# Optimization experiments

Measured on AMD Instinct MI355X. Metric: run time of the kernel, lower is better.

Reference implementation:

```python
import jax, jax.numpy as jnp
import numpy as np

PRED_WEIGHT = 1.0
GT_WEIGHT = 1.0
EPS = 1e-9
P = 16384
G = 16384


def setup_inputs() -> dict:
    key = jax.random.key(0)
    k1, k2, k3, k4 = jax.random.split(key, 4)
    return {
        "pred_points": jax.random.normal(k1, (P, 3), dtype=jnp.float32),
        "gt_points": jax.random.normal(k2, (G, 3), dtype=jnp.float32),
        "w_pred": jax.random.uniform(k3, (P,), dtype=jnp.float32),
        "w_gt": jax.random.uniform(k4, (G,), dtype=jnp.float32),
    }


def reference(pred_points, gt_points, w_pred, w_gt):
    # squared pairwise distances: ||p||^2 + ||g||^2 - 2 p.g, clamped at 0
    p2 = jnp.sum(pred_points * pred_points, axis=1)  # (P,)
    g2 = jnp.sum(gt_points * gt_points, axis=1)      # (G,)
    d2 = p2[:, None] + g2[None, :] - 2.0 * (pred_points @ gt_points.T)  # (P, G)
    d2 = jnp.maximum(d2, 0.0)
    min_pred = jnp.min(d2, axis=1)  # (P,)
    min_gt = jnp.min(d2, axis=0)    # (G,)
    weighted_pred = jnp.sum(w_pred * min_pred) / jnp.maximum(jnp.sum(w_pred), EPS)
    weighted_gt = jnp.sum(w_gt * min_gt) / jnp.maximum(jnp.sum(w_gt), EPS)
    return PRED_WEIGHT * weighted_pred + GT_WEIGHT * weighted_gt
```

## Files before the change

kernel.cpp:

```cpp
#include <hip/hip_runtime.h>
#include <math.h>


constexpr int NPTS  = 16384;
constexpr int BLOCK = 512;
constexpr int WAVES = BLOCK / 64;

constexpr int COLS_PER_BLOCK = 64;
constexpr int NCB = NPTS / COLS_PER_BLOCK;
constexpr int ROWS_PER_WAVE = NPTS / WAVES;
constexpr int ATILES = ROWS_PER_WAVE / 32;

typedef __attribute__((ext_vector_type(8)))  __bf16 bf16x8;
typedef __attribute__((ext_vector_type(16))) float  f32x16;

__device__ inline unsigned short f2bf(float f) {
    unsigned u = __float_as_uint(f);
    u += 0x7FFFu + ((u >> 16) & 1u);
    return (unsigned short)(u >> 16);
}
__device__ inline float bf2f(unsigned short h) {
    return __uint_as_float(((unsigned)h) << 16);
}
__device__ inline unsigned pk(unsigned short lo, unsigned short hi) {
    return (unsigned)lo | ((unsigned)hi << 16);
}

__global__ __launch_bounds__(256) void pack_init_kernel(
    const float* __restrict__ pred, const float* __restrict__ gt,
    uint4* __restrict__ Af, uint4* __restrict__ Bf,
    uint4* __restrict__ Ag, uint4* __restrict__ Bp)
{
    const unsigned short ONE = 0x3F80;
    int i = blockIdx.x * 256 + threadIdx.x;
    if (i >= NPTS) return;

    {
        float x = pred[3*i], y = pred[3*i+1], z = pred[3*i+2];
        unsigned short hx = f2bf(x), hy = f2bf(y), hz = f2bf(z);
        unsigned short lx = f2bf(x - bf2f(hx));
        unsigned short ly = f2bf(y - bf2f(hy));
        unsigned short lz = f2bf(z - bf2f(hz));
        float p2 = fmaf(x, x, fmaf(y, y, z * z));
        unsigned short sh = f2bf(p2), sl = f2bf(p2 - bf2f(sh));
        uint4 a0, a1, b0, b1;
        a0.x = pk(hx, hy); a0.y = pk(hz, lx); a0.z = pk(ly, lz); a0.w = pk(hx, hy);
        a1.x = pk(hz, sh); a1.y = pk(sl, ONE); a1.z = pk(ONE, lx); a1.w = pk(ly, lz);
        b0.x = pk(hx, hy); b0.y = pk(hz, hx); b0.z = pk(hy, hz); b0.w = pk(lx, ly);
        b1.x = pk(lz, ONE); b1.y = pk(ONE, sh); b1.z = pk(sl, lx); b1.w = pk(ly, lz);
        Af[i] = a0; Af[NPTS + i] = a1;
        Bp[i] = b0; Bp[NPTS + i] = b1;
    }
    {
        float gx = gt[3*i], gy = gt[3*i+1], gz = gt[3*i+2];
        float mx = -2.0f * gx, my = -2.0f * gy, mz = -2.0f * gz;
        unsigned short hx = f2bf(mx), hy = f2bf(my), hz = f2bf(mz);
        unsigned short lx = f2bf(mx - bf2f(hx));
        unsigned short ly = f2bf(my - bf2f(hy));
        unsigned short lz = f2bf(mz - bf2f(hz));
        float g2 = fmaf(gx, gx, fmaf(gy, gy, gz * gz));
        unsigned short sh = f2bf(g2), sl = f2bf(g2 - bf2f(sh));
        uint4 a0, a1, b0, b1;
        a0.x = pk(hx, hy); a0.y = pk(hz, lx); a0.z = pk(ly, lz); a0.w = pk(hx, hy);
        a1.x = pk(hz, sh); a1.y = pk(sl, ONE); a1.z = pk(ONE, lx); a1.w = pk(ly, lz);
        b0.x = pk(hx, hy); b0.y = pk(hz, hx); b0.z = pk(hy, hz); b0.w = pk(lx, ly);
        b1.x = pk(lz, ONE); b1.y = pk(ONE, sh); b1.z = pk(sl, lx); b1.w = pk(ly, lz);
        Ag[i] = a0; Ag[NPTS + i] = a1;
        Bf[i] = b0; Bf[NPTS + i] = b1;
    }
}

__device__ inline float tree16(const f32x16 a) {
    float m0 = fminf(fminf(a[0],  a[1]),  a[2]);
    float m1 = fminf(fminf(a[3],  a[4]),  a[5]);
    float m2 = fminf(fminf(a[6],  a[7]),  a[8]);
    float m3 = fminf(fminf(a[9],  a[10]), a[11]);
    float m4 = fminf(fminf(a[12], a[13]), a[14]);
    float m5 = fminf(fminf(m0, m1), m2);
    float m6 = fminf(fminf(m3, m4), a[15]);
    return fminf(m5, m6);
}

__global__ __launch_bounds__(BLOCK, 2) void chamfer_mfma_kernel(
    const uint4* __restrict__ Af, const uint4* __restrict__ Bf,
    const uint4* __restrict__ Ag, const uint4* __restrict__ Bp,
    const float* __restrict__ wpred, const float* __restrict__ wgt,
    float2* __restrict__ partials)
{
    const int tid  = threadIdx.x;
    const int wv   = tid >> 6;
    const int lane = tid & 63;
    const int half = lane >> 5;
    const int ln31 = lane & 31;

    const uint4* __restrict__ Aside;
    const uint4* __restrict__ Bside;
    const float* __restrict__ w;
    if (blockIdx.y == 0) { Aside = Af; Bside = Bf; w = wgt;   }
    else                 { Aside = Ag; Bside = Bp; w = wpred; }

    const int colBase = blockIdx.x * COLS_PER_BLOCK;

    bf16x8 bf0 = __builtin_bit_cast(bf16x8, Bside[half * NPTS + colBase + ln31]);
    bf16x8 bf1 = __builtin_bit_cast(bf16x8, Bside[half * NPTS + colBase + 32 + ln31]);

    const uint4* __restrict__ Ah = Aside + half * NPTS + wv * ROWS_PER_WAVE;

    const f32x16 zacc = {0.f,0.f,0.f,0.f, 0.f,0.f,0.f,0.f,
                         0.f,0.f,0.f,0.f, 0.f,0.f,0.f,0.f};

    float rm0 = INFINITY, rm1 = INFINITY;

    #pragma unroll 2
    for (int t = 0; t < ATILES; ++t) {
        bf16x8 af = __builtin_bit_cast(bf16x8, Ah[t * 32 + ln31]);
        f32x16 a0 = __builtin_amdgcn_mfma_f32_32x32x16_bf16(af, bf0, zacc, 0, 0, 0);
        f32x16 a1 = __builtin_amdgcn_mfma_f32_32x32x16_bf16(af, bf1, zacc, 0, 0, 0);
        rm0 = fminf(rm0, tree16(a0));
        rm1 = fminf(rm1, tree16(a1));
    }

    rm0 = fminf(rm0, __shfl_xor(rm0, 32, 64));
    rm1 = fminf(rm1, __shfl_xor(rm1, 32, 64));

    __shared__ unsigned int cmin[COLS_PER_BLOCK];
    if (tid < COLS_PER_BLOCK) cmin[tid] = 0x7F800000u;
    __syncthreads();
    if (half == 0) {
        atomicMin(&cmin[ln31],      __float_as_uint(fmaxf(rm0, 0.0f)));
        atomicMin(&cmin[32 + ln31], __float_as_uint(fmaxf(rm1, 0.0f)));
    }
    __syncthreads();

    if (tid < COLS_PER_BLOCK) {
        float v  = __uint_as_float(cmin[tid]);
        float wc = w[colBase + tid];
        float num = wc * v;
        float den = wc;
        #pragma unroll
        for (int off = 1; off < 64; off <<= 1) {
            num += __shfl_xor(num, off, 64);
            den += __shfl_xor(den, off, 64);
        }
        if (tid == 0)
            partials[blockIdx.y * NCB + blockIdx.x] = make_float2(num, den);
    }
}

__global__ __launch_bounds__(256) void finalize_kernel(
    const float2* __restrict__ partials, float* __restrict__ out)
{
    const int tid  = threadIdx.x;
    const int lane = tid & 63;
    const int wv   = tid >> 6;

    float2 p0 = partials[tid];
    float2 p1 = partials[NCB + tid];
    float ng = p0.x, dg = p0.y, np = p1.x, dp = p1.y;

    #pragma unroll
    for (int off = 1; off < 64; off <<= 1) {
        ng += __shfl_xor(ng, off, 64);
        dg += __shfl_xor(dg, off, 64);
        np += __shfl_xor(np, off, 64);
        dp += __shfl_xor(dp, off, 64);
    }
    __shared__ float sred[4][4];
    if (lane == 0) { sred[0][wv] = ng; sred[1][wv] = dg;
                     sred[2][wv] = np; sred[3][wv] = dp; }
    __syncthreads();
    if (tid == 0) {
        float NG = 0.f, DG = 0.f, NP = 0.f, DP = 0.f;
        #pragma unroll
        for (int k = 0; k < 4; ++k) {
            NG += sred[0][k]; DG += sred[1][k];
            NP += sred[2][k]; DP += sred[3][k];
        }
        out[0] = NP / fmaxf(DP, 1e-9f) + NG / fmaxf(DG, 1e-9f);
    }
}

extern "C" void kernel_launch(void* const* d_in, const int* in_sizes, int n_in,
                              void* d_out, int out_size, void* d_ws, size_t ws_size,
                              hipStream_t stream)
{
    const float* pred  = (const float*)d_in[0];
    const float* gt    = (const float*)d_in[1];
    const float* wpred = (const float*)d_in[2];
    const float* wgt   = (const float*)d_in[3];
    float* out = (float*)d_out;

    uint4* Af = (uint4*)d_ws;
    uint4* Bf = Af + 2 * NPTS;
    uint4* Ag = Bf + 2 * NPTS;
    uint4* Bp = Ag + 2 * NPTS;
    float2* partials = (float2*)(Bp + 2 * NPTS);

    pack_init_kernel<<<NPTS / 256, 256, 0, stream>>>(
        pred, gt, Af, Bf, Ag, Bp);

    chamfer_mfma_kernel<<<dim3(NCB, 2), BLOCK, 0, stream>>>(
        Af, Bf, Ag, Bp, wpred, wgt, partials);

    finalize_kernel<<<1, 256, 0, stream>>>(partials, out);
}
```

Baseline: 84.48 us.

## Widen chamfer block to 128 columns with 1024 threads and four MFMAs per A-tile

```diff
diff --git a/kernel.cpp b/kernel.cpp
--- a/kernel.cpp
+++ b/kernel.cpp
@@ -3,10 +3,10 @@
 
 
 constexpr int NPTS  = 16384;
-constexpr int BLOCK = 512;
+constexpr int BLOCK = 1024;
 constexpr int WAVES = BLOCK / 64;
 
-constexpr int COLS_PER_BLOCK = 64;
+constexpr int COLS_PER_BLOCK = 128;
 constexpr int NCB = NPTS / COLS_PER_BLOCK;
 constexpr int ROWS_PER_WAVE = NPTS / WAVES;
 constexpr int ATILES = ROWS_PER_WAVE / 32;
@@ -81,7 +81,7 @@
     return fminf(m5, m6);
 }
 
-__global__ __launch_bounds__(BLOCK, 2) void chamfer_mfma_kernel(
+__global__ __launch_bounds__(BLOCK) void chamfer_mfma_kernel(
     const uint4* __restrict__ Af, const uint4* __restrict__ Bf,
     const uint4* __restrict__ Ag, const uint4* __restrict__ Bp,
     const float* __restrict__ wpred, const float* __restrict__ wgt,
@@ -101,27 +101,36 @@
 
     const int colBase = blockIdx.x * COLS_PER_BLOCK;
 
-    bf16x8 bf0 = __builtin_bit_cast(bf16x8, Bside[half * NPTS + colBase + ln31]);
-    bf16x8 bf1 = __builtin_bit_cast(bf16x8, Bside[half * NPTS + colBase + 32 + ln31]);
+    const uint4* __restrict__ Bh = Bside + half * NPTS + colBase;
+    bf16x8 bf0 = __builtin_bit_cast(bf16x8, Bh[ln31]);
+    bf16x8 bf1 = __builtin_bit_cast(bf16x8, Bh[32 + ln31]);
+    bf16x8 bf2 = __builtin_bit_cast(bf16x8, Bh[64 + ln31]);
+    bf16x8 bf3 = __builtin_bit_cast(bf16x8, Bh[96 + ln31]);
 
     const uint4* __restrict__ Ah = Aside + half * NPTS + wv * ROWS_PER_WAVE;
 
     const f32x16 zacc = {0.f,0.f,0.f,0.f, 0.f,0.f,0.f,0.f,
                          0.f,0.f,0.f,0.f, 0.f,0.f,0.f,0.f};
 
-    float rm0 = INFINITY, rm1 = INFINITY;
+    float rm0 = INFINITY, rm1 = INFINITY, rm2 = INFINITY, rm3 = INFINITY;
 
     #pragma unroll 2
     for (int t = 0; t < ATILES; ++t) {
         bf16x8 af = __builtin_bit_cast(bf16x8, Ah[t * 32 + ln31]);
         f32x16 a0 = __builtin_amdgcn_mfma_f32_32x32x16_bf16(af, bf0, zacc, 0, 0, 0);
         f32x16 a1 = __builtin_amdgcn_mfma_f32_32x32x16_bf16(af, bf1, zacc, 0, 0, 0);
+        f32x16 a2 = __builtin_amdgcn_mfma_f32_32x32x16_bf16(af, bf2, zacc, 0, 0, 0);
+        f32x16 a3 = __builtin_amdgcn_mfma_f32_32x32x16_bf16(af, bf3, zacc, 0, 0, 0);
         rm0 = fminf(rm0, tree16(a0));
         rm1 = fminf(rm1, tree16(a1));
+        rm2 = fminf(rm2, tree16(a2));
+        rm3 = fminf(rm3, tree16(a3));
     }
 
     rm0 = fminf(rm0, __shfl_xor(rm0, 32, 64));
     rm1 = fminf(rm1, __shfl_xor(rm1, 32, 64));
+    rm2 = fminf(rm2, __shfl_xor(rm2, 32, 64));
+    rm3 = fminf(rm3, __shfl_xor(rm3, 32, 64));
 
     __shared__ unsigned int cmin[COLS_PER_BLOCK];
     if (tid < COLS_PER_BLOCK) cmin[tid] = 0x7F800000u;
@@ -129,9 +138,12 @@
     if (half == 0) {
         atomicMin(&cmin[ln31],      __float_as_uint(fmaxf(rm0, 0.0f)));
         atomicMin(&cmin[32 + ln31], __float_as_uint(fmaxf(rm1, 0.0f)));
-    }
-    __syncthreads();
-
+        atomicMin(&cmin[64 + ln31], __float_as_uint(fmaxf(rm2, 0.0f)));
+        atomicMin(&cmin[96 + ln31], __float_as_uint(fmaxf(rm3, 0.0f)));
+    }
+    __syncthreads();
+
+    __shared__ float psum[2][2];
     if (tid < COLS_PER_BLOCK) {
         float v  = __uint_as_float(cmin[tid]);
         float wc = w[colBase + tid];
@@ -142,12 +154,16 @@
             num += __shfl_xor(num, off, 64);
             den += __shfl_xor(den, off, 64);
         }
-        if (tid == 0)
-            partials[blockIdx.y * NCB + blockIdx.x] = make_float2(num, den);
-    }
-}
-
-__global__ __launch_bounds__(256) void finalize_kernel(
+        if (lane == 0) { psum[tid >> 6][0] = num; psum[tid >> 6][1] = den; }
+    }
+    __syncthreads();
+    if (tid == 0) {
+        partials[blockIdx.y * NCB + blockIdx.x] =
+            make_float2(psum[0][0] + psum[1][0], psum[0][1] + psum[1][1]);
+    }
+}
+
+__global__ __launch_bounds__(128) void finalize_kernel(
     const float2* __restrict__ partials, float* __restrict__ out)
 {
     const int tid  = threadIdx.x;
@@ -165,17 +181,15 @@
         np += __shfl_xor(np, off, 64);
         dp += __shfl_xor(dp, off, 64);
     }
-    __shared__ float sred[4][4];
+    __shared__ float sred[4][2];
     if (lane == 0) { sred[0][wv] = ng; sred[1][wv] = dg;
                      sred[2][wv] = np; sred[3][wv] = dp; }
     __syncthreads();
     if (tid == 0) {
-        float NG = 0.f, DG = 0.f, NP = 0.f, DP = 0.f;
-        #pragma unroll
-        for (int k = 0; k < 4; ++k) {
-            NG += sred[0][k]; DG += sred[1][k];
-            NP += sred[2][k]; DP += sred[3][k];
-        }
+        float NG = sred[0][0] + sred[0][1];
+        float DG = sred[1][0] + sred[1][1];
+        float NP = sred[2][0] + sred[2][1];
+        float DP = sred[3][0] + sred[3][1];
         out[0] = NP / fmaxf(DP, 1e-9f) + NG / fmaxf(DG, 1e-9f);
     }
 }
@@ -202,5 +216,5 @@
     chamfer_mfma_kernel<<<dim3(NCB, 2), BLOCK, 0, stream>>>(
         Af, Bf, Ag, Bp, wpred, wgt, partials);
 
-    finalize_kernel<<<1, 256, 0, stream>>>(partials, out);
-}
+    finalize_kernel<<<1, 128, 0, stream>>>(partials, out);
+}
```

After: 81.58 us (median of 2 runs). 1.04x faster.

## Split row range into slices with global atomic min and fused weighted finalize

Applied to the files above, without the earlier changes.

```diff
diff --git a/kernel.cpp b/kernel.cpp
--- a/kernel.cpp
+++ b/kernel.cpp
@@ -3,12 +3,14 @@
 
 
 constexpr int NPTS  = 16384;
-constexpr int BLOCK = 512;
+constexpr int BLOCK = 256;
 constexpr int WAVES = BLOCK / 64;
 
 constexpr int COLS_PER_BLOCK = 64;
 constexpr int NCB = NPTS / COLS_PER_BLOCK;
-constexpr int ROWS_PER_WAVE = NPTS / WAVES;
+constexpr int RSLICES = 4;
+constexpr int ROWS_PER_SLICE = NPTS / RSLICES;
+constexpr int ROWS_PER_WAVE = ROWS_PER_SLICE / WAVES;
 constexpr int ATILES = ROWS_PER_WAVE / 32;
 
 typedef __attribute__((ext_vector_type(8)))  __bf16 bf16x8;
@@ -29,7 +31,8 @@
 __global__ __launch_bounds__(256) void pack_init_kernel(
     const float* __restrict__ pred, const float* __restrict__ gt,
     uint4* __restrict__ Af, uint4* __restrict__ Bf,
-    uint4* __restrict__ Ag, uint4* __restrict__ Bp)
+    uint4* __restrict__ Ag, uint4* __restrict__ Bp,
+    unsigned int* __restrict__ minP, unsigned int* __restrict__ minG)
 {
     const unsigned short ONE = 0x3F80;
     int i = blockIdx.x * 256 + threadIdx.x;
@@ -68,6 +71,8 @@
         Ag[i] = a0; Ag[NPTS + i] = a1;
         Bf[i] = b0; Bf[NPTS + i] = b1;
     }
+    minP[i] = 0x7F800000u;
+    minG[i] = 0x7F800000u;
 }
 
 __device__ inline float tree16(const f32x16 a) {
@@ -81,11 +86,10 @@
     return fminf(m5, m6);
 }
 
-__global__ __launch_bounds__(BLOCK, 2) void chamfer_mfma_kernel(
+__global__ __launch_bounds__(BLOCK) void chamfer_mfma_kernel(
     const uint4* __restrict__ Af, const uint4* __restrict__ Bf,
     const uint4* __restrict__ Ag, const uint4* __restrict__ Bp,
-    const float* __restrict__ wpred, const float* __restrict__ wgt,
-    float2* __restrict__ partials)
+    unsigned int* __restrict__ minP, unsigned int* __restrict__ minG)
 {
     const int tid  = threadIdx.x;
     const int wv   = tid >> 6;
@@ -95,16 +99,18 @@
 
     const uint4* __restrict__ Aside;
     const uint4* __restrict__ Bside;
-    const float* __restrict__ w;
-    if (blockIdx.y == 0) { Aside = Af; Bside = Bf; w = wgt;   }
-    else                 { Aside = Ag; Bside = Bp; w = wpred; }
+    unsigned int* __restrict__ outMin;
+    if (blockIdx.z == 0) { Aside = Af; Bside = Bf; outMin = minG; }
+    else                 { Aside = Ag; Bside = Bp; outMin = minP; }
 
     const int colBase = blockIdx.x * COLS_PER_BLOCK;
-
-    bf16x8 bf0 = __builtin_bit_cast(bf16x8, Bside[half * NPTS + colBase + ln31]);
-    bf16x8 bf1 = __builtin_bit_cast(bf16x8, Bside[half * NPTS + colBase + 32 + ln31]);
-
-    const uint4* __restrict__ Ah = Aside + half * NPTS + wv * ROWS_PER_WAVE;
+    const int rowBase = blockIdx.y * ROWS_PER_SLICE + wv * ROWS_PER_WAVE;
+
+    const uint4* __restrict__ Bh = Bside + half * NPTS + colBase;
+    bf16x8 bf0 = __builtin_bit_cast(bf16x8, Bh[ln31]);
+    bf16x8 bf1 = __builtin_bit_cast(bf16x8, Bh[32 + ln31]);
+
+    const uint4* __restrict__ Ah = Aside + half * NPTS + rowBase;
 
     const f32x16 zacc = {0.f,0.f,0.f,0.f, 0.f,0.f,0.f,0.f,
                          0.f,0.f,0.f,0.f, 0.f,0.f,0.f,0.f};
@@ -132,49 +138,47 @@
     }
     __syncthreads();
 
-    if (tid < COLS_PER_BLOCK) {
-        float v  = __uint_as_float(cmin[tid]);
-        float wc = w[colBase + tid];
-        float num = wc * v;
-        float den = wc;
-        #pragma unroll
-        for (int off = 1; off < 64; off <<= 1) {
-            num += __shfl_xor(num, off, 64);
-            den += __shfl_xor(den, off, 64);
-        }
-        if (tid == 0)
-            partials[blockIdx.y * NCB + blockIdx.x] = make_float2(num, den);
-    }
-}
-
-__global__ __launch_bounds__(256) void finalize_kernel(
-    const float2* __restrict__ partials, float* __restrict__ out)
+    if (tid < COLS_PER_BLOCK)
+        atomicMin(&outMin[colBase + tid], cmin[tid]);
+}
+
+__global__ __launch_bounds__(1024) void finalize_kernel(
+    const unsigned int* __restrict__ minP,
+    const unsigned int* __restrict__ minG,
+    const float* __restrict__ wpred, const float* __restrict__ wgt,
+    float* __restrict__ out)
 {
     const int tid  = threadIdx.x;
     const int lane = tid & 63;
     const int wv   = tid >> 6;
 
-    float2 p0 = partials[tid];
-    float2 p1 = partials[NCB + tid];
-    float ng = p0.x, dg = p0.y, np = p1.x, dp = p1.y;
-
+    float np = 0.f, dp = 0.f, ng = 0.f, dg = 0.f;
+    #pragma unroll 4
+    for (int i = tid; i < NPTS; i += 1024) {
+        float v = __uint_as_float(minP[i]);
+        float w = wpred[i];
+        np = fmaf(w, v, np); dp += w;
+        float u = __uint_as_float(minG[i]);
+        float x = wgt[i];
+        ng = fmaf(x, u, ng); dg += x;
+    }
     #pragma unroll
     for (int off = 1; off < 64; off <<= 1) {
+        np += __shfl_xor(np, off, 64);
+        dp += __shfl_xor(dp, off, 64);
         ng += __shfl_xor(ng, off, 64);
         dg += __shfl_xor(dg, off, 64);
-        np += __shfl_xor(np, off, 64);
-        dp += __shfl_xor(dp, off, 64);
-    }
-    __shared__ float sred[4][4];
-    if (lane == 0) { sred[0][wv] = ng; sred[1][wv] = dg;
-                     sred[2][wv] = np; sred[3][wv] = dp; }
+    }
+    __shared__ float sred[4][16];
+    if (lane == 0) { sred[0][wv] = np; sred[1][wv] = dp;
+                     sred[2][wv] = ng; sred[3][wv] = dg; }
     __syncthreads();
     if (tid == 0) {
-        float NG = 0.f, DG = 0.f, NP = 0.f, DP = 0.f;
+        float NP = 0.f, DP = 0.f, NG = 0.f, DG = 0.f;
         #pragma unroll
-        for (int k = 0; k < 4; ++k) {
-            NG += sred[0][k]; DG += sred[1][k];
-            NP += sred[2][k]; DP += sred[3][k];
+        for (int k = 0; k < 16; ++k) {
+            NP += sred[0][k]; DP += sred[1][k];
+            NG += sred[2][k]; DG += sred[3][k];
         }
         out[0] = NP / fmaxf(DP, 1e-9f) + NG / fmaxf(DG, 1e-9f);
     }
@@ -194,13 +198,14 @@
     uint4* Bf = Af + 2 * NPTS;
     uint4* Ag = Bf + 2 * NPTS;
     uint4* Bp = Ag + 2 * NPTS;
-    float2* partials = (float2*)(Bp + 2 * NPTS);
+    unsigned int* minP = (unsigned int*)(Bp + 2 * NPTS);
+    unsigned int* minG = minP + NPTS;
 
     pack_init_kernel<<<NPTS / 256, 256, 0, stream>>>(
-        pred, gt, Af, Bf, Ag, Bp);
-
-    chamfer_mfma_kernel<<<dim3(NCB, 2), BLOCK, 0, stream>>>(
-        Af, Bf, Ag, Bp, wpred, wgt, partials);
-
-    finalize_kernel<<<1, 256, 0, stream>>>(partials, out);
-}
+        pred, gt, Af, Bf, Ag, Bp, minP, minG);
+
+    chamfer_mfma_kernel<<<dim3(NCB, RSLICES, 2), BLOCK, 0, stream>>>(
+        Af, Bf, Ag, Bp, minP, minG);
+
+    finalize_kernel<<<1, 1024, 0, stream>>>(minP, minG, wpred, wgt, out);
+}
```

New measurement: 93.66 us. 10.9% more time.
